# Kernel tuning notes

Hardware: AMD Instinct MI355X
Metric: run time of the kernel (lower is better)

The kernel has to match this reference:

```python
import jax, jax.numpy as jnp
import numpy as np

# Module hyperparameters (from init_kwargs)
NUM_NEURONS = 16384
BATCH = 2048  # processed sequentially, sharing neuron state
V_TH0 = 1.0
V_RESET = 0.0
TAU = 20.0
DT = 1.0
ETA = 0.1
NOISE_STD = 0.1
MIN_TH = 0.5
MAX_TH = 2.0
USE_ADAPTIVE = True
STOCHASTIC = True


def setup_inputs() -> dict:
    key = jax.random.key(0)
    k1, k2 = jax.random.split(key)
    input_current = jax.random.normal(k1, (BATCH, NUM_NEURONS), dtype=jnp.float32)
    # stochastic membrane noise, pre-sampled for determinism
    noise = NOISE_STD * jax.random.normal(k2, (BATCH, NUM_NEURONS), dtype=jnp.float32)
    if not STOCHASTIC:
        noise = jnp.zeros_like(noise)
    return {"input_current": input_current, "noise": noise}


def reference(input_current, noise):
    # Faithful to the torch wrapper: each batch row is fed through the SAME
    # LIFNeuronGroup sequentially, carrying membrane potential V and the
    # adaptive threshold V_th across rows -> lax.scan over the batch axis.
    n = input_current.shape[1]
    V0 = jnp.full((n,), V_RESET, dtype=jnp.float32)
    Vth0 = jnp.full((n,), V_TH0, dtype=jnp.float32)

    def step(carry, inp):
        V, Vth = carry
        I, nz = inp
        # leaky integration + noise injection (fused elementwise)
        V = V + (DT / TAU) * (I - V) + nz
        spikes = V >= Vth
        V = jnp.where(spikes, V_RESET, V)
        if USE_ADAPTIVE:
            Vth = jnp.clip(Vth + ETA * spikes.astype(jnp.float32), MIN_TH, MAX_TH)
        return (V, Vth), spikes.astype(jnp.float32)

    (_, _), out_spikes = jax.lax.scan(step, (V0, Vth0), (input_current, noise))
    return out_spikes  # [batch, num_neurons] binary float32
```

## Files before the change

kernel.cpp:

```cpp
#include <hip/hip_runtime.h>
#include <hip/hip_bf16.h>


constexpr int N = 16384;
constexpr int T = 2048;
constexpr int U = 16;

__global__ __launch_bounds__(64, 1)
void TorchLIFNeuronGroup_85152021610615_kernel(const float* __restrict__ I,
                                               const float* __restrict__ Z,
                                               float* __restrict__ O) {
    #pragma clang fp contract(off)
    const int n = blockIdx.x * 64 + threadIdx.x;
    const float* ip = I + n;
    const float* zp = Z + n;
    float* op = O + n;

    float V   = 0.0f;
    float Vth = 1.0f;

    float bi[U], bz[U];
    #pragma unroll
    for (int u = 0; u < U; ++u) {
        bi[u] = __builtin_nontemporal_load(ip + u * N);
        bz[u] = __builtin_nontemporal_load(zp + u * N);
    }

    for (int t0 = 0; t0 < T; t0 += U) {
        float ci[U], cz[U];
        const bool more = (t0 + U) < T;
        if (more) {
            #pragma unroll
            for (int u = 0; u < U; ++u) {
                ci[u] = __builtin_nontemporal_load(ip + (t0 + U + u) * N);
                cz[u] = __builtin_nontemporal_load(zp + (t0 + U + u) * N);
            }
        }

        #pragma unroll
        for (int u = 0; u < U; ++u) {
            float d  = bi[u] - V;
            float v1 = V + 0.05f * d;
            float v2 = v1 + bz[u];
            bool  s  = (v2 >= Vth);
            V = s ? 0.0f : v2;
            float nth = fminf(fmaxf(Vth + 0.1f, 0.5f), 2.0f);
            Vth = s ? nth : Vth;
            __builtin_nontemporal_store(s ? 1.0f : 0.0f, op + (t0 + u) * N);
        }

        if (more) {
            #pragma unroll
            for (int u = 0; u < U; ++u) { bi[u] = ci[u]; bz[u] = cz[u]; }
        }
    }
}

extern "C" void kernel_launch(void* const* d_in, const int* in_sizes, int n_in,
                              void* d_out, int out_size, void* d_ws, size_t ws_size,
                              hipStream_t stream) {
    const float* input_current = (const float*)d_in[0];
    const float* noise         = (const float*)d_in[1];
    float* out                 = (float*)d_out;

    TorchLIFNeuronGroup_85152021610615_kernel<<<N / 64, 64, 0, stream>>>(
        input_current, noise, out);
}
```

Before: 352.0 us.

## Deepen load prefetch into a multi-stage register ring buffer

Result: no change. 345.7 us (-1.8%).

```diff
diff --git a/kernel.cpp b/kernel.cpp
--- a/kernel.cpp
+++ b/kernel.cpp
@@ -1,10 +1,11 @@
 #include <hip/hip_runtime.h>
-#include <hip/hip_bf16.h>
 
 
 constexpr int N = 16384;
 constexpr int T = 2048;
-constexpr int U = 16;
+constexpr int U = 8;
+constexpr int D = 8;
+constexpr int C = T / U;
 
 __global__ __launch_bounds__(64, 1)
 void TorchLIFNeuronGroup_85152021610615_kernel(const float* __restrict__ I,
@@ -19,39 +20,45 @@
     float V   = 0.0f;
     float Vth = 1.0f;
 
-    float bi[U], bz[U];
+    float bi[D][U], bz[D][U];
+
     #pragma unroll
-    for (int u = 0; u < U; ++u) {
-        bi[u] = __builtin_nontemporal_load(ip + u * N);
-        bz[u] = __builtin_nontemporal_load(zp + u * N);
+    for (int d = 0; d < D - 1; ++d) {
+        #pragma unroll
+        for (int u = 0; u < U; ++u) {
+            bi[d][u] = __builtin_nontemporal_load(ip + (size_t)(d * U + u) * N);
+            bz[d][u] = __builtin_nontemporal_load(zp + (size_t)(d * U + u) * N);
+        }
     }
 
-    for (int t0 = 0; t0 < T; t0 += U) {
-        float ci[U], cz[U];
-        const bool more = (t0 + U) < T;
-        if (more) {
+    for (int sc = 0; sc < C; sc += D) {
+        #pragma unroll
+        for (int d = 0; d < D; ++d) {
+            const int chunk = sc + d;
+            const int pre   = chunk + (D - 1);
+            if (pre < C) {
+                const int slot = (d + D - 1) % D;
+                #pragma unroll
+                for (int u = 0; u < U; ++u) {
+                    bi[slot][u] = __builtin_nontemporal_load(ip + (size_t)(pre * U + u) * N);
+                    bz[slot][u] = __builtin_nontemporal_load(zp + (size_t)(pre * U + u) * N);
+                }
+            }
+            __builtin_amdgcn_sched_barrier(0);
+
             #pragma unroll
             for (int u = 0; u < U; ++u) {
-                ci[u] = __builtin_nontemporal_load(ip + (t0 + U + u) * N);
-                cz[u] = __builtin_nontemporal_load(zp + (t0 + U + u) * N);
+                float dd = bi[d][u] - V;
+                float v1 = V + 0.05f * dd;
+                float v2 = v1 + bz[d][u];
+                bool  s  = (v2 >= Vth);
+                V = s ? 0.0f : v2;
+                float nth = fminf(fmaxf(Vth + 0.1f, 0.5f), 2.0f);
+                Vth = s ? nth : Vth;
+                __builtin_nontemporal_store(s ? 1.0f : 0.0f,
+                                            op + (size_t)(chunk * U + u) * N);
             }
-        }
-
-        #pragma unroll
-        for (int u = 0; u < U; ++u) {
-            float d  = bi[u] - V;
-            float v1 = V + 0.05f * d;
-            float v2 = v1 + bz[u];
-            bool  s  = (v2 >= Vth);
-            V = s ? 0.0f : v2;
-            float nth = fminf(fmaxf(Vth + 0.1f, 0.5f), 2.0f);
-            Vth = s ? nth : Vth;
-            __builtin_nontemporal_store(s ? 1.0f : 0.0f, op + (t0 + u) * N);
-        }
-
-        if (more) {
-            #pragma unroll
-            for (int u = 0; u < U; ++u) { bi[u] = ci[u]; bz[u] = cz[u]; }
+            __builtin_amdgcn_sched_barrier(0);
         }
     }
 }
```

## Add producer wavefront streaming inputs into LDS ring for compute wavefront

Applied to the files above, without the earlier changes.

After: 418.9 us. 1.19x slower.

```diff
diff --git a/kernel.cpp b/kernel.cpp
--- a/kernel.cpp
+++ b/kernel.cpp
@@ -1,57 +1,117 @@
 #include <hip/hip_runtime.h>
-#include <hip/hip_bf16.h>
 
 
-constexpr int N = 16384;
-constexpr int T = 2048;
-constexpr int U = 16;
+constexpr int N  = 16384;
+constexpr int T  = 2048;
+constexpr int U  = 8;
+constexpr int NC = T / U;
+constexpr int R  = 16;
+constexpr int W  = 3;
 
-__global__ __launch_bounds__(64, 1)
+#define FLAG_LOAD(p)     __hip_atomic_load((p), __ATOMIC_RELAXED, __HIP_MEMORY_SCOPE_WORKGROUP)
+#define FLAG_STORE(p, v) __hip_atomic_store((p), (v), __ATOMIC_RELAXED, __HIP_MEMORY_SCOPE_WORKGROUP)
+
+__device__ __forceinline__ void gl_lds4(const float* g, float* l) {
+    __builtin_amdgcn_global_load_lds(
+        (const __attribute__((address_space(1))) void*)g,
+        (__attribute__((address_space(3))) void*)l, 4, 0, 0);
+}
+
+__global__
+__attribute__((amdgpu_flat_work_group_size(128, 128)))
 void TorchLIFNeuronGroup_85152021610615_kernel(const float* __restrict__ I,
                                                const float* __restrict__ Z,
                                                float* __restrict__ O) {
     #pragma clang fp contract(off)
-    const int n = blockIdx.x * 64 + threadIdx.x;
-    const float* ip = I + n;
-    const float* zp = Z + n;
-    float* op = O + n;
+    __shared__ float ring[R][2][U][64];
+    __shared__ int ready_flag;
+    __shared__ int cons_flag;
 
-    float V   = 0.0f;
-    float Vth = 1.0f;
+    if (threadIdx.x == 0) { ready_flag = -1; cons_flag = -1; }
+    __syncthreads();
 
-    float bi[U], bz[U];
-    #pragma unroll
-    for (int u = 0; u < U; ++u) {
-        bi[u] = __builtin_nontemporal_load(ip + u * N);
-        bz[u] = __builtin_nontemporal_load(zp + u * N);
-    }
+    if (threadIdx.x >= 64) {
+        const int lane = threadIdx.x - 64;
+        const float* gI = I + (size_t)blockIdx.x * 64 + lane;
+        const float* gZ = Z + (size_t)blockIdx.x * 64 + lane;
 
-    for (int t0 = 0; t0 < T; t0 += U) {
-        float ci[U], cz[U];
-        const bool more = (t0 + U) < T;
-        if (more) {
+        for (int k = 0; k < NC; ++k) {
+            if (k >= R) {
+                while (FLAG_LOAD(&cons_flag) < k - R) __builtin_amdgcn_s_sleep(1);
+            }
+            __asm__ volatile("" ::: "memory");
+            const int slot = k & (R - 1);
+            const size_t tb = (size_t)k * U * N;
             #pragma unroll
             for (int u = 0; u < U; ++u) {
-                ci[u] = __builtin_nontemporal_load(ip + (t0 + U + u) * N);
-                cz[u] = __builtin_nontemporal_load(zp + (t0 + U + u) * N);
+                gl_lds4(gI + tb + (size_t)u * N, &ring[slot][0][u][0]);
+                gl_lds4(gZ + tb + (size_t)u * N, &ring[slot][1][u][0]);
+            }
+            if (k >= W) {
+                __asm__ volatile("s_waitcnt vmcnt(48)" ::: "memory");
+                if (lane == 0) FLAG_STORE(&ready_flag, k - W);
             }
         }
+        __asm__ volatile("s_waitcnt vmcnt(0)" ::: "memory");
+        if (lane == 0) FLAG_STORE(&ready_flag, NC - 1);
 
+    } else {
+        const int lane = threadIdx.x;
+        float* op = O + (size_t)blockIdx.x * 64 + lane;
+
+        float V   = 0.0f;
+        float Vth = 1.0f;
+        float ai[U], az[U], bi[U], bz[U];
+
+        while (FLAG_LOAD(&ready_flag) < 0) __builtin_amdgcn_s_sleep(1);
+        __asm__ volatile("" ::: "memory");
         #pragma unroll
-        for (int u = 0; u < U; ++u) {
-            float d  = bi[u] - V;
-            float v1 = V + 0.05f * d;
-            float v2 = v1 + bz[u];
-            bool  s  = (v2 >= Vth);
-            V = s ? 0.0f : v2;
-            float nth = fminf(fmaxf(Vth + 0.1f, 0.5f), 2.0f);
-            Vth = s ? nth : Vth;
-            __builtin_nontemporal_store(s ? 1.0f : 0.0f, op + (t0 + u) * N);
-        }
+        for (int u = 0; u < U; ++u) { ai[u] = ring[0][0][u][lane]; az[u] = ring[0][1][u][lane]; }
 
-        if (more) {
+        for (int k = 0; k < NC; k += 2) {
+            while (FLAG_LOAD(&ready_flag) < k + 1) __builtin_amdgcn_s_sleep(1);
+            __asm__ volatile("" ::: "memory");
+            {
+                const int slot = (k + 1) & (R - 1);
+                #pragma unroll
+                for (int u = 0; u < U; ++u) { bi[u] = ring[slot][0][u][lane]; bz[u] = ring[slot][1][u][lane]; }
+            }
             #pragma unroll
-            for (int u = 0; u < U; ++u) { bi[u] = ci[u]; bz[u] = cz[u]; }
+            for (int u = 0; u < U; ++u) {
+                #pragma clang fp contract(off)
+                float d  = ai[u] - V;
+                float v1 = V + 0.05f * d;
+                float v2 = v1 + az[u];
+                bool  s  = (v2 >= Vth);
+                V = s ? 0.0f : v2;
+                float nth = fminf(fmaxf(Vth + 0.1f, 0.5f), 2.0f);
+                Vth = s ? nth : Vth;
+                op[(size_t)(k * U + u) * N] = s ? 1.0f : 0.0f;
+            }
+            __asm__ volatile("" ::: "memory");
+            if (lane == 0) FLAG_STORE(&cons_flag, k);
+
+            if (k + 2 < NC) {
+                while (FLAG_LOAD(&ready_flag) < k + 2) __builtin_amdgcn_s_sleep(1);
+                __asm__ volatile("" ::: "memory");
+                const int slot = (k + 2) & (R - 1);
+                #pragma unroll
+                for (int u = 0; u < U; ++u) { ai[u] = ring[slot][0][u][lane]; az[u] = ring[slot][1][u][lane]; }
+            }
+            #pragma unroll
+            for (int u = 0; u < U; ++u) {
+                #pragma clang fp contract(off)
+                float d  = bi[u] - V;
+                float v1 = V + 0.05f * d;
+                float v2 = v1 + bz[u];
+                bool  s  = (v2 >= Vth);
+                V = s ? 0.0f : v2;
+                float nth = fminf(fmaxf(Vth + 0.1f, 0.5f), 2.0f);
+                Vth = s ? nth : Vth;
+                op[(size_t)((k + 1) * U + u) * N] = s ? 1.0f : 0.0f;
+            }
+            __asm__ volatile("" ::: "memory");
+            if (lane == 0) FLAG_STORE(&cons_flag, k + 1);
         }
     }
 }
@@ -63,6 +123,6 @@
     const float* noise         = (const float*)d_in[1];
     float* out                 = (float*)d_out;
 
-    TorchLIFNeuronGroup_85152021610615_kernel<<<N / 64, 64, 0, stream>>>(
+    TorchLIFNeuronGroup_85152021610615_kernel<<<N / 64, 128, 0, stream>>>(
         input_current, noise, out);
 }
```
